# Performance work log

Hardware: AMD Instinct MI355X
Metric: run time of the kernel (lower is better)

Reference implementation:

```python
import jax, jax.numpy as jnp
import numpy as np
from jax import lax

NUM_HEADS = 4
EPS = 1e-12  # torch F.normalize eps


def _conv1x1(x, w):
    # x: [b, cin, h, w], w: [cout, cin] -> [b, cout, h, w]
    return jnp.einsum('bchw,oc->bohw', x, w)


def _dwconv3x3(x, w):
    # depthwise 3x3, padding=1; w: [C, 1, 3, 3]
    return lax.conv_general_dilated(
        x, w, window_strides=(1, 1), padding='SAME',
        feature_group_count=x.shape[1],
        dimension_numbers=('NCHW', 'OIHW', 'NCHW'))


def _l2norm(x):
    # F.normalize over last dim
    n = jnp.linalg.norm(x, axis=-1, keepdims=True)
    return x / jnp.maximum(n, EPS)


def _mdta(q, k, v, temperature, h, w):
    # q,k,v: [b, C, h, w] -> channel attention per head -> [b, C, h, w]
    b, c, _, _ = q.shape
    ch = c // NUM_HEADS
    def to_heads(t):
        return t.reshape(b, NUM_HEADS, ch, h * w)  # b head c (hw)
    qh, kh, vh = to_heads(q), to_heads(k), to_heads(v)
    qh = _l2norm(qh)
    kh = _l2norm(kh)
    attn = jnp.einsum('bhcn,bhdn->bhcd', qh, kh) * temperature  # [b,head,ch,ch]
    attn = jax.nn.softmax(attn, axis=-1)
    out = jnp.einsum('bhcd,bhdn->bhcn', attn, vh)
    return out.reshape(b, c, h, w)


def setup_inputs() -> dict:
    key = jax.random.key(0)
    ks = jax.random.split(key, 7)
    b, c, h, w = 2, 192, 128, 128
    return {
        'x': jax.random.normal(ks[0], (b, c, h, w), jnp.float32),
        'y': jax.random.normal(ks[1], (b, c, h, w), jnp.float32),
        'qkv_w': jax.random.normal(ks[2], (3 * c, c), jnp.float32) * (1.0 / np.sqrt(c)),
        'dw_w': jax.random.normal(ks[3], (3 * c, 1, 3, 3), jnp.float32) * (1.0 / 3.0),
        'kv_w': jax.random.normal(ks[4], (2 * c, c), jnp.float32) * (1.0 / np.sqrt(c)),
        'proj_w': jax.random.normal(ks[5], (c, c), jnp.float32) * (1.0 / np.sqrt(c)),
        'temperature': jnp.ones((NUM_HEADS, 1, 1), jnp.float32),
    }


def reference(x, y, qkv_w, dw_w, kv_w, proj_w, temperature):
    b, c, h, w = x.shape
    qkv = _dwconv3x3(_conv1x1(x, qkv_w), dw_w)
    q, k, v = jnp.split(qkv, 3, axis=1)
    # intra_fusion_attention(q, y): kv from y, channel attention with q
    kv = _conv1x1(y, kv_w)
    k2, v2 = jnp.split(kv, 2, axis=1)
    q = _mdta(q, k2, v2, temperature, h, w)
    out = _mdta(q, k, v, temperature, h, w)
    return _conv1x1(out, proj_w)
```

## Files before the change

kernel.cpp:

```cpp
#include <hip/hip_runtime.h>
#include <hip/hip_bf16.h>

#define HW 16384
#define IMGW 128
#define Bsz 2
#define Cc 192
#define NH 4
#define CH 48
static const size_t CP = (size_t)Cc * HW;

typedef __attribute__((ext_vector_type(4))) float f32x4;
typedef __attribute__((ext_vector_type(8))) short short8;
typedef __attribute__((ext_vector_type(8))) unsigned short bf16x8;
typedef __attribute__((ext_vector_type(4))) unsigned short bf16x4;

__device__ __forceinline__ unsigned short f2bf(float f) {
  __hip_bfloat16 h = __float2bfloat16(f);
  return *reinterpret_cast<unsigned short*>(&h);
}
__device__ __forceinline__ float bf2f(unsigned short u) {
  union { unsigned int i; float f; } v;
  v.i = (unsigned int)u << 16;
  return v.f;
}

#define NWQKV (576 * 192)
#define NWKV  (384 * 192)
__global__ __launch_bounds__(256) void cast_weights_kernel(
    const float* __restrict__ qkv_w, const float* __restrict__ kv_w,
    unsigned short* __restrict__ wqkv, unsigned short* __restrict__ wkv) {
  int i = blockIdx.x * 256 + threadIdx.x;
  if (i < NWQKV) wqkv[i] = f2bf(qkv_w[i]);
  else if (i < NWQKV + NWKV) wkv[i - NWQKV] = f2bf(kv_w[i - NWQKV]);
}

#define APAD 200

template <int INKIND, int OUTBF16>
__global__ __launch_bounds__(256) void conv_mfma_kernel(
    const void* __restrict__ src, size_t src_bstride,
    const unsigned short* __restrict__ wb, size_t wstride,
    void* __restrict__ outv, int Cout) {
  __shared__ __align__(16) short As[64 * APAD];
  __shared__ __align__(16) short Bs[64 * APAD];
  unsigned int* As32 = (unsigned int*)As;
  const int b = blockIdx.z;
  const int hw0 = blockIdx.x * 64;
  const int tid = threadIdx.x;
  const int lane = tid & 63, wid = tid >> 6;
  const int wm = wid & 1, wn = wid >> 1;
  const int l = tid & 15, pp0 = tid >> 4;
  const unsigned short* wbbase = wb + (size_t)b * wstride;
  const int NT = Cout >> 6;

  #pragma unroll
  for (int kp = 0; kp < 3; ++kp) {
    #pragma unroll
    for (int it = 0; it < 2; ++it) {
      int pp = pp0 + 16 * it;
      int c0 = kp * 64 + 2 * pp;
      if (INKIND == 1) {
        const float* r0 = (const float*)src + (size_t)b * src_bstride +
                          (size_t)c0 * HW + hw0 + l * 4;
        f32x4 v0 = *(const f32x4*)r0;
        f32x4 v1 = *(const f32x4*)(r0 + HW);
        #pragma unroll
        for (int i = 0; i < 4; ++i)
          As32[(l * 4 + i) * (APAD / 2) + kp * 32 + pp] =
              (unsigned int)f2bf(v0[i]) | ((unsigned int)f2bf(v1[i]) << 16);
      } else {
        const unsigned short* r0 = (const unsigned short*)src +
                                   (size_t)b * src_bstride +
                                   (size_t)c0 * HW + hw0 + l * 4;
        bf16x4 v0 = *(const bf16x4*)r0;
        bf16x4 v1 = *(const bf16x4*)(r0 + HW);
        #pragma unroll
        for (int i = 0; i < 4; ++i)
          As32[(l * 4 + i) * (APAD / 2) + kp * 32 + pp] =
              (unsigned int)v0[i] | ((unsigned int)v1[i] << 16);
      }
    }
  }

  for (int ot = 0; ot < NT; ++ot) {
    const unsigned short* wbb = wbbase + (size_t)(ot * 64) * Cc;
    #pragma unroll
    for (int p = 0; p < 6; ++p) {
      int i = tid + p * 256;
      int row = i / 24, cc = i - (i / 24) * 24;
      *(short8*)&Bs[row * APAD + cc * 8] =
          *(const short8*)(wbb + (size_t)row * Cc + cc * 8);
    }
    __syncthreads();
    f32x4 acc[2][2] = {};
    #pragma unroll
    for (int ks = 0; ks < 6; ++ks) {
      short8 bfrag[2];
      #pragma unroll
      for (int fn = 0; fn < 2; ++fn)
        bfrag[fn] = *(short8*)&Bs[(wn * 32 + fn * 16 + (lane & 15)) * APAD +
                                  ks * 32 + (lane >> 4) * 8];
      #pragma unroll
      for (int fm = 0; fm < 2; ++fm) {
        short8 afrag = *(short8*)&As[(wm * 32 + fm * 16 + (lane & 15)) * APAD +
                                     ks * 32 + (lane >> 4) * 8];
        #pragma unroll
        for (int fn = 0; fn < 2; ++fn)
          acc[fm][fn] = __builtin_amdgcn_mfma_f32_16x16x32_bf16(
              afrag, bfrag[fn], acc[fm][fn], 0, 0, 0);
      }
    }
    __syncthreads();
    #pragma unroll
    for (int fm = 0; fm < 2; ++fm)
      #pragma unroll
      for (int fn = 0; fn < 2; ++fn) {
        int o = ot * 64 + wn * 32 + fn * 16 + (lane & 15);
        int hw = hw0 + wm * 32 + fm * 16 + ((lane >> 4) << 2);
        if (OUTBF16) {
          bf16x4 u;
          #pragma unroll
          for (int r = 0; r < 4; ++r) u[r] = f2bf(acc[fm][fn][r]);
          *(bf16x4*)&((unsigned short*)outv)[((size_t)b * Cout + o) * HW + hw] = u;
        } else {
          *(f32x4*)&((float*)outv)[((size_t)b * Cout + o) * HW + hw] = acc[fm][fn];
        }
      }
  }
}

__global__ __launch_bounds__(256) void dwconv_kernel(
    const unsigned short* __restrict__ in, const float* __restrict__ wgt,
    unsigned short* __restrict__ out, int Ctot) {
  const int b = blockIdx.z, ch = blockIdx.y;
  const int p0 = blockIdx.x * 2048 + threadIdx.x * 8;
  const int y = p0 >> 7, x0 = p0 & 127;
  const unsigned short* ip = in + ((size_t)b * Ctot + ch) * HW;
  const float* wp = wgt + ch * 9;
  float acc[8] = {};
  #pragma unroll
  for (int dy = -1; dy <= 1; ++dy) {
    int yy = y + dy;
    if (yy < 0 || yy > IMGW - 1) continue;
    const unsigned short* rp = ip + yy * IMGW;
    float r[10];
    bf16x8 mid = *(const bf16x8*)&rp[x0];
    #pragma unroll
    for (int e = 0; e < 8; ++e) r[e + 1] = bf2f(mid[e]);
    r[0] = (x0 > 0) ? bf2f(rp[x0 - 1]) : 0.f;
    r[9] = (x0 < 120) ? bf2f(rp[x0 + 8]) : 0.f;
    #pragma unroll
    for (int dx = 0; dx < 3; ++dx) {
      float wv = wp[(dy + 1) * 3 + dx];
      #pragma unroll
      for (int e = 0; e < 8; ++e) acc[e] += wv * r[e + dx];
    }
  }
  bf16x8 u;
  #pragma unroll
  for (int e = 0; e < 8; ++e) u[e] = f2bf(acc[e]);
  *(bf16x8*)&out[((size_t)b * Ctot + ch) * HW + p0] = u;
}

__global__ __launch_bounds__(256) void norm3_kernel(
    const unsigned short* __restrict__ qkvb,
    const unsigned short* __restrict__ kvb, float* __restrict__ inv) {
  const int kind = blockIdx.x / 384;
  const int row = blockIdx.x % 384;
  const int b = row / Cc, r = row % Cc;
  const unsigned short* p;
  if (kind == 0)      p = qkvb + (size_t)b * 3 * CP + (size_t)r * HW;
  else if (kind == 1) p = kvb + (size_t)b * 2 * CP + (size_t)r * HW;
  else                p = qkvb + (size_t)b * 3 * CP + CP + (size_t)r * HW;
  float s = 0.f;
  for (int i = threadIdx.x * 8; i < HW; i += 2048) {
    bf16x8 u = *(const bf16x8*)&p[i];
    #pragma unroll
    for (int j = 0; j < 8; ++j) {
      float v = bf2f(u[j]);
      s += v * v;
    }
  }
  #pragma unroll
  for (int off = 32; off; off >>= 1) s += __shfl_down(s, off);
  __shared__ float red[4];
  if ((threadIdx.x & 63) == 0) red[threadIdx.x >> 6] = s;
  __syncthreads();
  if (threadIdx.x == 0) {
    float t = red[0] + red[1] + red[2] + red[3];
    inv[blockIdx.x] = 1.f / fmaxf(sqrtf(t), 1e-12f);
  }
}

#define PK 136
#define NCHUNK 16
__global__ __launch_bounds__(256) void gram_mfma_kernel(
    const unsigned short* __restrict__ qkvb,
    const unsigned short* __restrict__ kvb, float* __restrict__ spart) {
  __shared__ __align__(16) char lds_raw[4 * 2304 * 4];
  short* Qs = (short*)lds_raw;
  short* Ks = Qs + 48 * PK;
  float* Rs = (float*)lds_raw;
  const int pair = blockIdx.z;
  const int bh = blockIdx.y, b = bh >> 2, hd = bh & 3;
  const int n0 = blockIdx.x * 1024;
  const int tid = threadIdx.x, lane = tid & 63, wid = tid >> 6;
  const unsigned short *ap, *bp;
  size_t as_, bs_;
  if (pair == 0)      { ap = qkvb;      as_ = 3 * CP; bp = kvb;       bs_ = 2 * CP; }
  else if (pair == 1) { ap = kvb + CP;  as_ = 2 * CP; bp = qkvb + CP; bs_ = 3 * CP; }
  else                { ap = kvb + CP;  as_ = 2 * CP; bp = kvb + CP;  bs_ = 2 * CP; }
  const unsigned short* qb = ap + (size_t)b * as_ + (size_t)(hd * CH) * HW + n0;
  const unsigned short* kb = bp + (size_t)b * bs_ + (size_t)(hd * CH) * HW + n0;
  f32x4 acc[3][3] = {};
  #pragma unroll 1
  for (int it = 0; it < 8; ++it) {
    #pragma unroll
    for (int p = 0; p < 3; ++p) {
      int c = tid + p * 256;
      int row = c >> 4, col = c & 15;
      *(short8*)&Qs[row * PK + col * 8] =
          *(const short8*)(qb + (size_t)row * HW + it * 128 + col * 8);
      *(short8*)&Ks[row * PK + col * 8] =
          *(const short8*)(kb + (size_t)row * HW + it * 128 + col * 8);
    }
    __syncthreads();
    short8 af[3], bfr[3];
    #pragma unroll
    for (int t = 0; t < 3; ++t) {
      af[t]  = *(short8*)&Qs[(t * 16 + (lane & 15)) * PK + wid * 32 + (lane >> 4) * 8];
      bfr[t] = *(short8*)&Ks[(t * 16 + (lane & 15)) * PK + wid * 32 + (lane >> 4) * 8];
    }
    #pragma unroll
    for (int mt = 0; mt < 3; ++mt)
      #pragma unroll
      for (int nt = 0; nt < 3; ++nt)
        acc[mt][nt] = __builtin_amdgcn_mfma_f32_16x16x32_bf16(
            af[mt], bfr[nt], acc[mt][nt], 0, 0, 0);
    __syncthreads();
  }
  #pragma unroll
  for (int mt = 0; mt < 3; ++mt)
    #pragma unroll
    for (int nt = 0; nt < 3; ++nt)
      #pragma unroll
      for (int r = 0; r < 4; ++r) {
        int i = mt * 16 + ((lane >> 4) << 2) + r;
        int j = nt * 16 + (lane & 15);
        Rs[wid * 2304 + i * 48 + j] = acc[mt][nt][r];
      }
  __syncthreads();
  float* sp = spart + ((size_t)(pair * 8 + bh) * NCHUNK + blockIdx.x) * 2304;
  for (int e = tid; e < 2304; e += 256)
    sp[e] = Rs[e] + Rs[2304 + e] + Rs[2 * 2304 + e] + Rs[3 * 2304 + e];
}

__global__ __launch_bounds__(256) void gram_reduce_kernel(
    const float* __restrict__ spart, float* __restrict__ G) {
  int idx = blockIdx.x * 256 + threadIdx.x;
  if (idx >= 3 * 8 * 2304) return;
  int pb = idx / 2304;
  int e = idx - pb * 2304;
  const float* sp = spart + (size_t)pb * NCHUNK * 2304 + e;
  float s = 0.f;
  #pragma unroll
  for (int c = 0; c < NCHUNK; ++c) s += sp[(size_t)c * 2304];
  G[idx] = s;
}

__global__ __launch_bounds__(256) void finalize_a2_kernel(
    const float* __restrict__ G, const float* __restrict__ inv,
    const float* __restrict__ temp, float* __restrict__ attn2) {
  __shared__ float A1[2304], GVV[2304], GVK[2304], S2[2304];
  __shared__ float invq1[48];
  const int bh = blockIdx.x, b = bh >> 2, hd = bh & 3;
  const int tid = threadIdx.x;
  const float tp = temp[hd];
  const float* invQ  = inv;
  const float* invK2 = inv + 384;
  const float* invK  = inv + 768;
  for (int e = tid; e < 2304; e += 256) {
    int i = e / 48, j = e - i * 48;
    A1[e] = G[(size_t)(0 * 8 + bh) * 2304 + e] *
            invQ[b * Cc + hd * CH + i] * invK2[b * Cc + hd * CH + j] * tp;
    GVV[e] = G[(size_t)(2 * 8 + bh) * 2304 + e];
    GVK[e] = G[(size_t)(1 * 8 + bh) * 2304 + e];
  }
  __syncthreads();
  if (tid < 192) {
    const int i = tid >> 2, g = tid & 3;
    float v[12];
    float m = -1e30f;
    #pragma unroll
    for (int k = 0; k < 12; ++k) {
      v[k] = A1[i * 48 + g * 12 + k];
      m = fmaxf(m, v[k]);
    }
    m = fmaxf(m, __shfl_xor(m, 1));
    m = fmaxf(m, __shfl_xor(m, 2));
    float sum = 0.f;
    #pragma unroll
    for (int k = 0; k < 12; ++k) {
      v[k] = expf(v[k] - m);
      sum += v[k];
    }
    sum += __shfl_xor(sum, 1);
    sum += __shfl_xor(sum, 2);
    float r = 1.f / sum;
    #pragma unroll
    for (int k = 0; k < 12; ++k) A1[i * 48 + g * 12 + k] = v[k] * r;
  }
  __syncthreads();
  const int ti = tid >> 4, tj = tid & 15;
  {
    float c[3][3] = {};
    #pragma unroll 4
    for (int d = 0; d < 48; ++d) {
      float a0 = A1[ti * 48 + d], a1 = A1[(ti + 16) * 48 + d],
            a2 = A1[(ti + 32) * 48 + d];
      float b0 = GVV[d * 48 + tj], b1 = GVV[d * 48 + tj + 16],
            b2 = GVV[d * 48 + tj + 32];
      c[0][0] += a0 * b0; c[0][1] += a0 * b1; c[0][2] += a0 * b2;
      c[1][0] += a1 * b0; c[1][1] += a1 * b1; c[1][2] += a1 * b2;
      c[2][0] += a2 * b0; c[2][1] += a2 * b1; c[2][2] += a2 * b2;
    }
    #pragma unroll
    for (int ii = 0; ii < 3; ++ii) {
      float p = 0.f;
      #pragma unroll
      for (int jj = 0; jj < 3; ++jj)
        p += c[ii][jj] * A1[(ti + 16 * ii) * 48 + tj + 16 * jj];
      p += __shfl_xor(p, 1);
      p += __shfl_xor(p, 2);
      p += __shfl_xor(p, 4);
      p += __shfl_xor(p, 8);
      if (tj == 0)
        invq1[ti + 16 * ii] = 1.f / fmaxf(sqrtf(fmaxf(p, 0.f)), 1e-12f);
    }
  }
  __syncthreads();
  {
    float s[3][3] = {};
    #pragma unroll 4
    for (int d = 0; d < 48; ++d) {
      float a0 = A1[ti * 48 + d], a1 = A1[(ti + 16) * 48 + d],
            a2 = A1[(ti + 32) * 48 + d];
      float b0 = GVK[d * 48 + tj], b1 = GVK[d * 48 + tj + 16],
            b2 = GVK[d * 48 + tj + 32];
      s[0][0] += a0 * b0; s[0][1] += a0 * b1; s[0][2] += a0 * b2;
      s[1][0] += a1 * b0; s[1][1] += a1 * b1; s[1][2] += a1 * b2;
      s[2][0] += a2 * b0; s[2][1] += a2 * b1; s[2][2] += a2 * b2;
    }
    #pragma unroll
    for (int ii = 0; ii < 3; ++ii)
      #pragma unroll
      for (int jj = 0; jj < 3; ++jj) {
        int i = ti + 16 * ii, j = tj + 16 * jj;
        S2[i * 48 + j] = s[ii][jj] * invq1[i] *
                         invK[b * Cc + hd * CH + j] * tp;
      }
  }
  __syncthreads();
  if (tid < 192) {
    const int i = tid >> 2, g = tid & 3;
    float v[12];
    float m = -1e30f;
    #pragma unroll
    for (int k = 0; k < 12; ++k) {
      v[k] = S2[i * 48 + g * 12 + k];
      m = fmaxf(m, v[k]);
    }
    m = fmaxf(m, __shfl_xor(m, 1));
    m = fmaxf(m, __shfl_xor(m, 2));
    float sum = 0.f;
    #pragma unroll
    for (int k = 0; k < 12; ++k) {
      v[k] = expf(v[k] - m);
      sum += v[k];
    }
    sum += __shfl_xor(sum, 1);
    sum += __shfl_xor(sum, 2);
    float r = 1.f / sum;
    #pragma unroll
    for (int k = 0; k < 12; ++k)
      attn2[(size_t)bh * 2304 + i * 48 + g * 12 + k] = v[k] * r;
  }
}

__global__ __launch_bounds__(192) void mproj_kernel(
    const float* __restrict__ P, const float* __restrict__ attn2,
    unsigned short* __restrict__ Mb) {
  const int b = blockIdx.y, o = blockIdx.x;
  const int c = threadIdx.x;
  const int hd = c / 48, j = c - hd * 48;
  const float* prow = P + (size_t)o * Cc + hd * 48;
  const float* arow = attn2 + (size_t)(b * 4 + hd) * 2304 + j;
  float s = 0.f;
  #pragma unroll 8
  for (int i = 0; i < 48; ++i) s += prow[i] * arow[(size_t)i * 48];
  Mb[((size_t)b * Cc + o) * Cc + c] = f2bf(s);
}

extern "C" void kernel_launch(void* const* d_in, const int* in_sizes, int n_in,
                              void* d_out, int out_size, void* d_ws, size_t ws_size,
                              hipStream_t stream) {
  const float* x      = (const float*)d_in[0];
  const float* y      = (const float*)d_in[1];
  const float* qkv_w  = (const float*)d_in[2];
  const float* dw_w   = (const float*)d_in[3];
  const float* kv_w   = (const float*)d_in[4];
  const float* proj_w = (const float*)d_in[5];
  const float* temp   = (const float*)d_in[6];
  float* out = (float*)d_out;
  float* ws  = (float*)d_ws;

  const size_t SF = (size_t)Bsz * CP;
  unsigned short* qkvb   = (unsigned short*)ws;
  unsigned short* kvb    = (unsigned short*)(ws + 3 * SF / 2);
  unsigned short* qkvpre = (unsigned short*)(ws + 5 * SF / 2);
  float* inv   = ws + 4 * SF;
  float* spart = inv + 1152;
  float* G     = spart + (size_t)3 * 8 * NCHUNK * 2304;
  float* attn2 = G + 3 * 8 * 2304;
  unsigned short* Mb   = (unsigned short*)(attn2 + 8 * 2304);
  unsigned short* wqkv = Mb + (size_t)Bsz * Cc * Cc;
  unsigned short* wkv  = wqkv + NWQKV;

  dim3 blk(256);

  cast_weights_kernel<<<dim3((NWQKV + NWKV + 255) / 256), blk, 0, stream>>>(
      qkv_w, kv_w, wqkv, wkv);

  conv_mfma_kernel<1, 1><<<dim3(HW / 64, 1, Bsz), blk, 0, stream>>>(
      x, CP, wqkv, 0, qkvpre, 3 * Cc);
  dwconv_kernel<<<dim3(HW / 2048, 3 * Cc, Bsz), blk, 0, stream>>>(
      qkvpre, dw_w, qkvb, 3 * Cc);
  conv_mfma_kernel<1, 1><<<dim3(HW / 64, 1, Bsz), blk, 0, stream>>>(
      y, CP, wkv, 0, kvb, 2 * Cc);

  norm3_kernel<<<dim3(3 * 384), blk, 0, stream>>>(qkvb, kvb, inv);

  gram_mfma_kernel<<<dim3(NCHUNK, 8, 3), blk, 0, stream>>>(qkvb, kvb, spart);
  gram_reduce_kernel<<<dim3(216), blk, 0, stream>>>(spart, G);

  finalize_a2_kernel<<<dim3(8), blk, 0, stream>>>(G, inv, temp, attn2);
  mproj_kernel<<<dim3(Cc, Bsz), dim3(192), 0, stream>>>(proj_w, attn2, Mb);

  conv_mfma_kernel<2, 0><<<dim3(HW / 64, 1, Bsz), blk, 0, stream>>>(
      qkvb + 2 * CP, 3 * CP, Mb, (size_t)Cc * Cc, out, Cc);
}
```

Measured before the change: 117.3 us.

## Fuse row norms into Gram kernel and projection into finalize kernel

Computes the squared L2 norms of Q, K2 and K inside the Gram MFMA kernel from data it already loads, writing per-chunk partials that the reduce kernel folds into inverse norms. This removes the separate norm3 pass over three large bf16 tensors. The attn2×proj_w product moves into the finalize kernel using bf16-cast weights in LDS, which removes the mproj launch and the attn2 round trip. In exchange the Gram kernel does extra ALU work for two of its three pairs, and the finalize kernel runs only 8 blocks doing serial work, so its latency grows.

```diff
diff --git a/kernel.cpp b/kernel.cpp
--- a/kernel.cpp
+++ b/kernel.cpp
@@ -162,41 +162,12 @@
   *(bf16x8*)&out[((size_t)b * Ctot + ch) * HW + p0] = u;
 }
 
-__global__ __launch_bounds__(256) void norm3_kernel(
-    const unsigned short* __restrict__ qkvb,
-    const unsigned short* __restrict__ kvb, float* __restrict__ inv) {
-  const int kind = blockIdx.x / 384;
-  const int row = blockIdx.x % 384;
-  const int b = row / Cc, r = row % Cc;
-  const unsigned short* p;
-  if (kind == 0)      p = qkvb + (size_t)b * 3 * CP + (size_t)r * HW;
-  else if (kind == 1) p = kvb + (size_t)b * 2 * CP + (size_t)r * HW;
-  else                p = qkvb + (size_t)b * 3 * CP + CP + (size_t)r * HW;
-  float s = 0.f;
-  for (int i = threadIdx.x * 8; i < HW; i += 2048) {
-    bf16x8 u = *(const bf16x8*)&p[i];
-    #pragma unroll
-    for (int j = 0; j < 8; ++j) {
-      float v = bf2f(u[j]);
-      s += v * v;
-    }
-  }
-  #pragma unroll
-  for (int off = 32; off; off >>= 1) s += __shfl_down(s, off);
-  __shared__ float red[4];
-  if ((threadIdx.x & 63) == 0) red[threadIdx.x >> 6] = s;
-  __syncthreads();
-  if (threadIdx.x == 0) {
-    float t = red[0] + red[1] + red[2] + red[3];
-    inv[blockIdx.x] = 1.f / fmaxf(sqrtf(t), 1e-12f);
-  }
-}
-
 #define PK 136
 #define NCHUNK 16
 __global__ __launch_bounds__(256) void gram_mfma_kernel(
     const unsigned short* __restrict__ qkvb,
-    const unsigned short* __restrict__ kvb, float* __restrict__ spart) {
+    const unsigned short* __restrict__ kvb, float* __restrict__ spart,
+    float* __restrict__ spartN) {
   __shared__ __align__(16) char lds_raw[4 * 2304 * 4];
   short* Qs = (short*)lds_raw;
   short* Ks = Qs + 48 * PK;
@@ -213,16 +184,37 @@
   const unsigned short* qb = ap + (size_t)b * as_ + (size_t)(hd * CH) * HW + n0;
   const unsigned short* kb = bp + (size_t)b * bs_ + (size_t)(hd * CH) * HW + n0;
   f32x4 acc[3][3] = {};
+  float sqA[3] = {}, sqB[3] = {};
   #pragma unroll 1
   for (int it = 0; it < 8; ++it) {
     #pragma unroll
     for (int p = 0; p < 3; ++p) {
       int c = tid + p * 256;
       int row = c >> 4, col = c & 15;
-      *(short8*)&Qs[row * PK + col * 8] =
-          *(const short8*)(qb + (size_t)row * HW + it * 128 + col * 8);
-      *(short8*)&Ks[row * PK + col * 8] =
-          *(const short8*)(kb + (size_t)row * HW + it * 128 + col * 8);
+      short8 vq = *(const short8*)(qb + (size_t)row * HW + it * 128 + col * 8);
+      short8 vk = *(const short8*)(kb + (size_t)row * HW + it * 128 + col * 8);
+      *(short8*)&Qs[row * PK + col * 8] = vq;
+      *(short8*)&Ks[row * PK + col * 8] = vk;
+      if (pair == 0) {
+        float aq = 0.f, ak = 0.f;
+        #pragma unroll
+        for (int j = 0; j < 8; ++j) {
+          float q = bf2f((unsigned short)vq[j]);
+          float k = bf2f((unsigned short)vk[j]);
+          aq += q * q;
+          ak += k * k;
+        }
+        sqA[p] += aq;
+        sqB[p] += ak;
+      } else if (pair == 1) {
+        float ak = 0.f;
+        #pragma unroll
+        for (int j = 0; j < 8; ++j) {
+          float k = bf2f((unsigned short)vk[j]);
+          ak += k * k;
+        }
+        sqB[p] += ak;
+      }
     }
     __syncthreads();
     short8 af[3], bfr[3];
@@ -239,6 +231,28 @@
             af[mt], bfr[nt], acc[mt][nt], 0, 0, 0);
     __syncthreads();
   }
+  if (pair < 2) {
+    #pragma unroll
+    for (int p = 0; p < 3; ++p)
+      #pragma unroll
+      for (int off = 1; off < 16; off <<= 1) {
+        if (pair == 0) sqA[p] += __shfl_xor(sqA[p], off);
+        sqB[p] += __shfl_xor(sqB[p], off);
+      }
+    if ((tid & 15) == 0) {
+      int r0 = tid >> 4;
+      float* np = spartN + ((size_t)bh * NCHUNK + blockIdx.x) * 144;
+      #pragma unroll
+      for (int p = 0; p < 3; ++p) {
+        if (pair == 0) {
+          np[r0 + 16 * p] = sqA[p];
+          np[48 + r0 + 16 * p] = sqB[p];
+        } else {
+          np[96 + r0 + 16 * p] = sqB[p];
+        }
+      }
+    }
+  }
   #pragma unroll
   for (int mt = 0; mt < 3; ++mt)
     #pragma unroll
@@ -255,23 +269,40 @@
     sp[e] = Rs[e] + Rs[2304 + e] + Rs[2 * 2304 + e] + Rs[3 * 2304 + e];
 }
 
-__global__ __launch_bounds__(256) void gram_reduce_kernel(
-    const float* __restrict__ spart, float* __restrict__ G) {
+__global__ __launch_bounds__(256) void reduce_kernel(
+    const float* __restrict__ spart, const float* __restrict__ spartN,
+    float* __restrict__ G, float* __restrict__ inv) {
   int idx = blockIdx.x * 256 + threadIdx.x;
-  if (idx >= 3 * 8 * 2304) return;
-  int pb = idx / 2304;
-  int e = idx - pb * 2304;
-  const float* sp = spart + (size_t)pb * NCHUNK * 2304 + e;
-  float s = 0.f;
-  #pragma unroll
-  for (int c = 0; c < NCHUNK; ++c) s += sp[(size_t)c * 2304];
-  G[idx] = s;
-}
-
-__global__ __launch_bounds__(256) void finalize_a2_kernel(
+  if (idx < 3 * 8 * 2304) {
+    int pb = idx / 2304;
+    int e = idx - pb * 2304;
+    const float* sp = spart + (size_t)pb * NCHUNK * 2304 + e;
+    float s = 0.f;
+    #pragma unroll
+    for (int c = 0; c < NCHUNK; ++c) s += sp[(size_t)c * 2304];
+    G[idx] = s;
+  } else if (idx < 3 * 8 * 2304 + 1152) {
+    int t = idx - 3 * 8 * 2304;
+    int kind = t / 384;
+    int row = t - kind * 384;
+    int b = row / 192;
+    int rr = row - b * 192;
+    int hd = rr / 48, r = rr - hd * 48;
+    int bh = b * 4 + hd;
+    const float* np = spartN + (size_t)bh * NCHUNK * 144 + kind * 48 + r;
+    float s = 0.f;
+    #pragma unroll
+    for (int c = 0; c < NCHUNK; ++c) s += np[c * 144];
+    inv[t] = 1.f / fmaxf(sqrtf(s), 1e-12f);
+  }
+}
+
+__global__ __launch_bounds__(256) void finalize_kernel(
     const float* __restrict__ G, const float* __restrict__ inv,
-    const float* __restrict__ temp, float* __restrict__ attn2) {
+    const float* __restrict__ temp, const float* __restrict__ proj_w,
+    unsigned short* __restrict__ Mb) {
   __shared__ float A1[2304], GVV[2304], GVK[2304], S2[2304];
+  __shared__ unsigned short Pb[192 * 48];
   __shared__ float invq1[48];
   const int bh = blockIdx.x, b = bh >> 2, hd = bh & 3;
   const int tid = threadIdx.x;
@@ -279,6 +310,10 @@
   const float* invQ  = inv;
   const float* invK2 = inv + 384;
   const float* invK  = inv + 768;
+  for (int e = tid; e < 192 * 48; e += 256) {
+    int o = e / 48, i = e - (e / 48) * 48;
+    Pb[e] = f2bf(proj_w[(size_t)o * Cc + hd * 48 + i]);
+  }
   for (int e = tid; e < 2304; e += 256) {
     int i = e / 48, j = e - i * 48;
     A1[e] = G[(size_t)(0 * 8 + bh) * 2304 + e] *
@@ -382,23 +417,31 @@
     sum += __shfl_xor(sum, 2);
     float r = 1.f / sum;
     #pragma unroll
-    for (int k = 0; k < 12; ++k)
-      attn2[(size_t)bh * 2304 + i * 48 + g * 12 + k] = v[k] * r;
-  }
-}
-
-__global__ __launch_bounds__(192) void mproj_kernel(
-    const float* __restrict__ P, const float* __restrict__ attn2,
-    unsigned short* __restrict__ Mb) {
-  const int b = blockIdx.y, o = blockIdx.x;
-  const int c = threadIdx.x;
-  const int hd = c / 48, j = c - hd * 48;
-  const float* prow = P + (size_t)o * Cc + hd * 48;
-  const float* arow = attn2 + (size_t)(b * 4 + hd) * 2304 + j;
-  float s = 0.f;
-  #pragma unroll 8
-  for (int i = 0; i < 48; ++i) s += prow[i] * arow[(size_t)i * 48];
-  Mb[((size_t)b * Cc + o) * Cc + c] = f2bf(s);
+    for (int k = 0; k < 12; ++k) S2[i * 48 + g * 12 + k] = v[k] * r;
+  }
+  __syncthreads();
+  {
+    float macc[12][3] = {};
+    #pragma unroll 4
+    for (int d = 0; d < 48; ++d) {
+      float b0 = S2[d * 48 + tj], b1 = S2[d * 48 + tj + 16],
+            b2 = S2[d * 48 + tj + 32];
+      #pragma unroll
+      for (int rr = 0; rr < 12; ++rr) {
+        float a = bf2f(Pb[(rr * 16 + ti) * 48 + d]);
+        macc[rr][0] += a * b0;
+        macc[rr][1] += a * b1;
+        macc[rr][2] += a * b2;
+      }
+    }
+    #pragma unroll
+    for (int rr = 0; rr < 12; ++rr)
+      #pragma unroll
+      for (int cc = 0; cc < 3; ++cc) {
+        int o = rr * 16 + ti, j = tj + 16 * cc;
+        Mb[((size_t)b * Cc + o) * Cc + hd * 48 + j] = f2bf(macc[rr][cc]);
+      }
+  }
 }
 
 extern "C" void kernel_launch(void* const* d_in, const int* in_sizes, int n_in,
@@ -418,11 +461,11 @@
   unsigned short* qkvb   = (unsigned short*)ws;
   unsigned short* kvb    = (unsigned short*)(ws + 3 * SF / 2);
   unsigned short* qkvpre = (unsigned short*)(ws + 5 * SF / 2);
-  float* inv   = ws + 4 * SF;
-  float* spart = inv + 1152;
-  float* G     = spart + (size_t)3 * 8 * NCHUNK * 2304;
-  float* attn2 = G + 3 * 8 * 2304;
-  unsigned short* Mb   = (unsigned short*)(attn2 + 8 * 2304);
+  float* inv    = ws + 4 * SF;
+  float* spart  = inv + 1152;
+  float* spartN = spart + (size_t)3 * 8 * NCHUNK * 2304;
+  float* G      = spartN + (size_t)8 * NCHUNK * 144;
+  unsigned short* Mb   = (unsigned short*)(G + 3 * 8 * 2304);
   unsigned short* wqkv = Mb + (size_t)Bsz * Cc * Cc;
   unsigned short* wkv  = wqkv + NWQKV;
 
@@ -438,13 +481,12 @@
   conv_mfma_kernel<1, 1><<<dim3(HW / 64, 1, Bsz), blk, 0, stream>>>(
       y, CP, wkv, 0, kvb, 2 * Cc);
 
-  norm3_kernel<<<dim3(3 * 384), blk, 0, stream>>>(qkvb, kvb, inv);
-
-  gram_mfma_kernel<<<dim3(NCHUNK, 8, 3), blk, 0, stream>>>(qkvb, kvb, spart);
-  gram_reduce_kernel<<<dim3(216), blk, 0, stream>>>(spart, G);
-
-  finalize_a2_kernel<<<dim3(8), blk, 0, stream>>>(G, inv, temp, attn2);
-  mproj_kernel<<<dim3(Cc, Bsz), dim3(192), 0, stream>>>(proj_w, attn2, Mb);
+  gram_mfma_kernel<<<dim3(NCHUNK, 8, 3), blk, 0, stream>>>(
+      qkvb, kvb, spart, spartN);
+  reduce_kernel<<<dim3((3 * 8 * 2304 + 1152 + 255) / 256), blk, 0, stream>>>(
+      spart, spartN, G, inv);
+
+  finalize_kernel<<<dim3(8), blk, 0, stream>>>(G, inv, temp, proj_w, Mb);
 
   conv_mfma_kernel<2, 0><<<dim3(HW / 64, 1, Bsz), blk, 0, stream>>>(
       qkvb + 2 * CP, 3 * CP, Mb, (size_t)Cc * Cc, out, Cc);
```

Result: slower. 119.8 us (+2.1%).
